# Kernel optimization log

Hardware: AMD Instinct MI355X
Metric: run time of the kernel (lower is better)

The kernel has to match this reference:

```python
import jax, jax.numpy as jnp
import numpy as np
import math

D_MODEL = 1024
NUM_HEADS = 16
BATCH = 2
SEQ = 2048

def setup_inputs() -> dict:
    key = jax.random.key(0)
    ks = jax.random.split(key, 9)
    s = 1.0 / math.sqrt(D_MODEL)
    inp = {
        "X": jax.random.normal(ks[0], (BATCH, SEQ, D_MODEL), dtype=jnp.float32),
        "Wq": jax.random.uniform(ks[1], (D_MODEL, D_MODEL), jnp.float32, -s, s),
        "bq": jax.random.uniform(ks[2], (D_MODEL,), jnp.float32, -s, s),
        "Wk": jax.random.uniform(ks[3], (D_MODEL, D_MODEL), jnp.float32, -s, s),
        "bk": jax.random.uniform(ks[4], (D_MODEL,), jnp.float32, -s, s),
        "Wv": jax.random.uniform(ks[5], (D_MODEL, D_MODEL), jnp.float32, -s, s),
        "bv": jax.random.uniform(ks[6], (D_MODEL,), jnp.float32, -s, s),
        "Wo": jax.random.uniform(ks[7], (D_MODEL, D_MODEL), jnp.float32, -s, s),
        "bo": jax.random.uniform(ks[8], (D_MODEL,), jnp.float32, -s, s),
    }
    return inp

def reference(X, Wq, bq, Wk, bk, Wv, bv, Wo, bo):
    B, S, D = X.shape
    H = NUM_HEADS
    dk = D // H
    # QKV projections (Linear: x @ W.T + b; here W stored as [in, out] so x @ W + b)
    q = X @ Wq + bq
    k = X @ Wk + bk
    v = X @ Wv + bv
    # split heads -> [B, H, S, dk]
    q = q.reshape(B, S, H, dk).transpose(0, 2, 1, 3)
    k = k.reshape(B, S, H, dk).transpose(0, 2, 1, 3)
    v = v.reshape(B, S, H, dk).transpose(0, 2, 1, 3)
    scores = jnp.einsum("bhqd,bhkd->bhqk", q, k) / math.sqrt(dk)
    weights = jax.nn.softmax(scores, axis=-1)
    attn = jnp.einsum("bhqk,bhkd->bhqd", weights, v)
    concat = attn.transpose(0, 2, 1, 3).reshape(B, S, D)
    return concat @ Wo + bo
```

## Files before the change

kernel.cpp:

```cpp
#include <hip/hip_runtime.h>
#include <stdint.h>

#define D_MODEL 1024
#define NH      16
#define DKH     64
#define BATCH   2
#define SEQ     2048
#define M_TOK   (BATCH*SEQ)

typedef __attribute__((ext_vector_type(8))) short bf16x8;
typedef __attribute__((ext_vector_type(4))) float f32x4;

__device__ __forceinline__ uint16_t f2b(float f) {
  uint32_t u = __builtin_bit_cast(uint32_t, f);
  return (uint16_t)((u + 0x7FFFu + ((u >> 16) & 1u)) >> 16);
}

__device__ __forceinline__ void gl2lds16(const uint16_t* g, uint16_t* l) {
  __builtin_amdgcn_global_load_lds(
      (const __attribute__((address_space(1))) void*)g,
      (__attribute__((address_space(3))) void*)l, 16, 0, 0);
}

__global__ void convx(const float* __restrict__ X, uint16_t* __restrict__ Xb) {
  int i = (blockIdx.x * 256 + threadIdx.x) * 8;
  float4 a = *(const float4*)(X + i);
  float4 b = *(const float4*)(X + i + 4);
  uint16_t tmp[8] = {f2b(a.x), f2b(a.y), f2b(a.z), f2b(a.w),
                     f2b(b.x), f2b(b.y), f2b(b.z), f2b(b.w)};
  *(uint4*)(Xb + i) = *(const uint4*)tmp;
}

__global__ void wtrans(const float* __restrict__ W0, const float* __restrict__ W1,
                       const float* __restrict__ W2, const float* __restrict__ W3,
                       uint16_t* __restrict__ T0, uint16_t* __restrict__ T1,
                       uint16_t* __restrict__ T2, uint16_t* __restrict__ T3) {
  __shared__ float tile[32][33];
  int z = blockIdx.z;
  const float* W = (z == 0) ? W0 : (z == 1) ? W1 : (z == 2) ? W2 : W3;
  uint16_t*    T = (z == 0) ? T0 : (z == 1) ? T1 : (z == 2) ? T2 : T3;
  int k0 = blockIdx.x * 32, n0 = blockIdx.y * 32;
  int tx = threadIdx.x, ty = threadIdx.y;
  tile[ty][tx] = W[(size_t)(k0 + ty) * D_MODEL + n0 + tx];
  __syncthreads();
  T[(size_t)(n0 + ty) * D_MODEL + k0 + tx] = f2b(tile[tx][ty]);
}

template <bool SWAP>
__device__ __forceinline__ void gemm_core(const uint16_t* __restrict__ A,
                                          const uint16_t* __restrict__ BT,
                                          uint16_t* As, uint16_t* Bs,
                                          int m0, int n0, int kBeg, int kEnd,
                                          f32x4 (&acc)[4][4]) {
  const int t    = threadIdx.x;
  const int lane = t & 63;
  const int qi   = lane & 15, g = lane >> 4;
  const int wm   = (t >> 7) & 1;
  const int wn   = (t >> 6) & 1;
  const int srow = t >> 2;
  const int sc   = (t & 3) ^ ((t >> 3) & 3);
  const int wbase = t & 192;
  const int rch  = (g ^ ((qi >> 1) & 3)) * 8;

  const uint16_t* Ag = A  + (size_t)(m0 + srow) * D_MODEL + sc * 8;
  const uint16_t* Bg = BT + (size_t)(n0 + srow) * D_MODEL + sc * 8;

#pragma unroll
  for (int j = 0; j < 2; j++) {
    gl2lds16(Ag + (size_t)j * 64 * D_MODEL + kBeg, As + (j * 256 + wbase) * 8);
    gl2lds16(Bg + (size_t)j * 64 * D_MODEL + kBeg, Bs + (j * 256 + wbase) * 8);
  }

  int cur = 0;
  for (int k0 = kBeg; k0 < kEnd; k0 += 32) {
    __syncthreads();
    int kn = k0 + 32;
    if (kn < kEnd) {
      int nb = (cur ^ 1) * 4096;
#pragma unroll
      for (int j = 0; j < 2; j++) {
        gl2lds16(Ag + (size_t)j * 64 * D_MODEL + kn, As + nb + (j * 256 + wbase) * 8);
        gl2lds16(Bg + (size_t)j * 64 * D_MODEL + kn, Bs + nb + (j * 256 + wbase) * 8);
      }
    }
    const uint16_t* Ab = As + cur * 4096;
    const uint16_t* Bb = Bs + cur * 4096;
    bf16x8 af[4], bf[4];
#pragma unroll
    for (int i = 0; i < 4; i++) {
      af[i] = *(const bf16x8*)(Ab + (wm * 64 + i * 16 + qi) * 32 + rch);
      bf[i] = *(const bf16x8*)(Bb + (wn * 64 + i * 16 + qi) * 32 + rch);
    }
#pragma unroll
    for (int i = 0; i < 4; i++)
#pragma unroll
      for (int j = 0; j < 4; j++)
        acc[i][j] = SWAP
          ? __builtin_amdgcn_mfma_f32_16x16x32_bf16(bf[j], af[i], acc[i][j], 0, 0, 0)
          : __builtin_amdgcn_mfma_f32_16x16x32_bf16(af[i], bf[j], acc[i][j], 0, 0, 0);
    cur ^= 1;
  }
}

__global__ __launch_bounds__(256) void qkv_gemm(
    const uint16_t* __restrict__ Xb,
    const uint16_t* __restrict__ WqT, const uint16_t* __restrict__ WkT,
    const uint16_t* __restrict__ WvT,
    const float* __restrict__ bq, const float* __restrict__ bk,
    const float* __restrict__ bv,
    uint16_t* __restrict__ Qo, uint16_t* __restrict__ Ko, uint16_t* __restrict__ Vt) {
  __shared__ __align__(16) uint16_t smem[17408];
  uint16_t* As = smem;
  uint16_t* Bs = smem + 8192;
  uint16_t* T  = smem;
  const int z = blockIdx.z;
  const uint16_t* BT  = (z == 0) ? WqT : (z == 1) ? WkT : WvT;
  const float*   bias = (z == 0) ? bq  : (z == 1) ? bk  : bv;
  const int m0 = blockIdx.y * 128, n0 = blockIdx.x * 128;
  const int lane = threadIdx.x & 63, qi = lane & 15, g = lane >> 4;
  const int wm = (threadIdx.x >> 7) & 1, wn = (threadIdx.x >> 6) & 1;
  const float l2e = 1.4426950408889634f * 0.125f;

  const f32x4 ZERO = {0.f, 0.f, 0.f, 0.f};
  f32x4 acc[4][4];
#pragma unroll
  for (int i = 0; i < 4; i++)
#pragma unroll
    for (int j = 0; j < 4; j++) acc[i][j] = ZERO;

  if (z == 2) {
    gemm_core<false>(Xb, BT, As, Bs, m0, n0, 0, D_MODEL, acc);
    __syncthreads();
#pragma unroll
    for (int i = 0; i < 4; i++) {
      int tok = wm * 64 + i * 16 + g * 4;
#pragma unroll
      for (int j = 0; j < 4; j++) {
        int ch = wn * 64 + j * 16 + qi;
        float bb = bias[n0 + ch];
        uint32_t lo = (uint32_t)f2b(acc[i][j][0] + bb) | ((uint32_t)f2b(acc[i][j][1] + bb) << 16);
        uint32_t hi = (uint32_t)f2b(acc[i][j][2] + bb) | ((uint32_t)f2b(acc[i][j][3] + bb) << 16);
        uint2 pk = {lo, hi};
        *(uint2*)(T + ch * 136 + tok) = pk;
      }
    }
    __syncthreads();
    {
      int ch = threadIdx.x >> 1, sh = threadIdx.x & 1;
      const uint16_t* src = T + ch * 136 + sh * 64;
      int bidx = m0 >> 11;
      uint16_t* dst = Vt + ((size_t)(bidx * D_MODEL + n0 + ch)) * SEQ + (m0 & 2047) + sh * 64;
#pragma unroll
      for (int u = 0; u < 8; u++)
        *(uint4*)(dst + u * 8) = *(const uint4*)(src + u * 8);
    }
  } else {
    gemm_core<true>(Xb, BT, As, Bs, m0, n0, 0, D_MODEL, acc);
    uint16_t* O = z ? Ko : Qo;
    const float osc = (z == 0) ? l2e : 1.0f;
#pragma unroll
    for (int i = 0; i < 4; i++) {
      size_t tok = m0 + wm * 64 + i * 16 + qi;
#pragma unroll
      for (int j = 0; j < 4; j++) {
        int ch = n0 + wn * 64 + j * 16 + g * 4;
        float4 bb = *(const float4*)(bias + ch);
        uint32_t lo = (uint32_t)f2b((acc[i][j][0] + bb.x) * osc) |
                      ((uint32_t)f2b((acc[i][j][1] + bb.y) * osc) << 16);
        uint32_t hi = (uint32_t)f2b((acc[i][j][2] + bb.z) * osc) |
                      ((uint32_t)f2b((acc[i][j][3] + bb.w) * osc) << 16);
        uint2 pk = {lo, hi};
        *(uint2*)(O + tok * D_MODEL + ch) = pk;
      }
    }
  }
}

__global__ __launch_bounds__(256) void oproj_gemm(
    const uint16_t* __restrict__ Ab, const uint16_t* __restrict__ WoT,
    const float* __restrict__ bo, float* __restrict__ out) {
  __shared__ __align__(16) uint16_t As[8192];
  __shared__ __align__(16) uint16_t Bs[4096];
  const int t = threadIdx.x;
  const int lane = t & 63, qi = lane & 15, g = lane >> 4;
  const int wm = (t >> 7) & 1;
  const int wn = (t >> 6) & 1;
  const int srow = t >> 2;
  const int sc = (t & 3) ^ ((t >> 3) & 3);
  const int wbase = t & 192;
  const int rch = (g ^ ((qi >> 1) & 3)) * 8;
  const int m0 = blockIdx.y * 128, n0 = blockIdx.x * 64;

  const uint16_t* Ag = Ab  + (size_t)(m0 + srow) * D_MODEL + sc * 8;
  const uint16_t* Bg = WoT + (size_t)(n0 + srow) * D_MODEL + sc * 8;

  const f32x4 ZERO = {0.f, 0.f, 0.f, 0.f};
  f32x4 acc[4][2];
#pragma unroll
  for (int i = 0; i < 4; i++)
#pragma unroll
    for (int j = 0; j < 2; j++) acc[i][j] = ZERO;

  gl2lds16(Ag, As + wbase * 8);
  gl2lds16(Ag + (size_t)64 * D_MODEL, As + (256 + wbase) * 8);
  gl2lds16(Bg, Bs + wbase * 8);

  int cur = 0;
  for (int k0 = 0; k0 < D_MODEL; k0 += 32) {
    __syncthreads();
    int kn = k0 + 32;
    if (kn < D_MODEL) {
      int nbA = (cur ^ 1) * 4096, nbB = (cur ^ 1) * 2048;
      gl2lds16(Ag + kn, As + nbA + wbase * 8);
      gl2lds16(Ag + (size_t)64 * D_MODEL + kn, As + nbA + (256 + wbase) * 8);
      gl2lds16(Bg + kn, Bs + nbB + wbase * 8);
    }
    const uint16_t* Abuf = As + cur * 4096;
    const uint16_t* Bbuf = Bs + cur * 2048;
    bf16x8 af[4], bf[2];
#pragma unroll
    for (int i = 0; i < 4; i++)
      af[i] = *(const bf16x8*)(Abuf + (wm * 64 + i * 16 + qi) * 32 + rch);
#pragma unroll
    for (int j = 0; j < 2; j++)
      bf[j] = *(const bf16x8*)(Bbuf + (wn * 32 + j * 16 + qi) * 32 + rch);
#pragma unroll
    for (int i = 0; i < 4; i++)
#pragma unroll
      for (int j = 0; j < 2; j++)
        acc[i][j] = __builtin_amdgcn_mfma_f32_16x16x32_bf16(bf[j], af[i], acc[i][j], 0, 0, 0);
    cur ^= 1;
  }

#pragma unroll
  for (int i = 0; i < 4; i++) {
    size_t tok = m0 + wm * 64 + i * 16 + qi;
#pragma unroll
    for (int j = 0; j < 2; j++) {
      int ch = n0 + wn * 32 + j * 16 + g * 4;
      float4 bb = *(const float4*)(bo + ch);
      float4 o = {acc[i][j][0] + bb.x, acc[i][j][1] + bb.y,
                  acc[i][j][2] + bb.z, acc[i][j][3] + bb.w};
      *(float4*)(out + tok * D_MODEL + ch) = o;
    }
  }
}

__global__ __launch_bounds__(512, 2) void attn_fwd(
    const uint16_t* __restrict__ Q, const uint16_t* __restrict__ K,
    const uint16_t* __restrict__ Vt, uint16_t* __restrict__ O) {
  __shared__ __align__(16) uint16_t sm[32768];
  uint16_t* Ps = sm + 16384;

  const int t = threadIdx.x, lane = t & 63, w = t >> 6;
  const int g = lane >> 4, qi = lane & 15;
  const int rch = (g ^ ((qi >> 1) & 3)) * 8;
  const int key = qi & 7;
  const int q0 = blockIdx.y * 256;
  const int bh = blockIdx.x, b = bh >> 4, h = bh & 15;
  const uint16_t* Qp = Q + (size_t)b * SEQ * D_MODEL + h * DKH;
  const uint16_t* Kp = K + (size_t)b * SEQ * D_MODEL + h * DKH;
  const uint16_t* Vp = Vt + (size_t)bh * DKH * SEQ;

  const int tt = t & 255, hs = t >> 8;
  const int srow = tt >> 2;
  const int sc = (tt & 3) ^ ((tt >> 3) & 3);
  const int wbase = tt & 192;

  bf16x8 qf[2][2];
#pragma unroll
  for (int i = 0; i < 2; i++) {
    const uint16_t* Qr = Qp + (size_t)(q0 + w * 32 + i * 16 + qi) * D_MODEL + g * 8;
    qf[0][i] = *(const bf16x8*)(Qr);
    qf[1][i] = *(const bf16x8*)(Qr + 32);
  }

  gl2lds16(Kp + (size_t)srow * D_MODEL + hs * 32 + sc * 8,
           sm + hs * 2048 + wbase * 8);
  gl2lds16(Vp + (size_t)srow * SEQ + hs * 32 + sc * 8,
           sm + 8192 + hs * 2048 + wbase * 8);
  __syncthreads();

  float lsum[2] = {0.f, 0.f};
  const f32x4 ZERO = {0.f, 0.f, 0.f, 0.f};
  f32x4 oaccT[4][2];
#pragma unroll
  for (int d = 0; d < 4; d++)
#pragma unroll
    for (int i = 0; i < 2; i++) oaccT[d][i] = ZERO;

  int cur = 0;
  for (int kt = 0; kt < SEQ / 64; kt++) {
    if (kt + 1 < SEQ / 64) {
      int nb = (cur ^ 1) * 4096;
      gl2lds16(Kp + (size_t)((kt + 1) * 64 + srow) * D_MODEL + hs * 32 + sc * 8,
               sm + nb + hs * 2048 + wbase * 8);
      gl2lds16(Vp + (size_t)srow * SEQ + (kt + 1) * 64 + hs * 32 + sc * 8,
               sm + 8192 + nb + hs * 2048 + wbase * 8);
    }
    const uint16_t* Kb = sm + cur * 4096;
    const uint16_t* Vb = sm + 8192 + cur * 4096;

    f32x4 sacc[4][2];
#pragma unroll
    for (int j = 0; j < 4; j++)
#pragma unroll
      for (int i = 0; i < 2; i++) sacc[j][i] = ZERO;
#pragma unroll
    for (int ks = 0; ks < 2; ks++) {
      const uint16_t* Ksb = Kb + ks * 2048;
      bf16x8 kf[4];
#pragma unroll
      for (int j = 0; j < 4; j++)
        kf[j] = *(const bf16x8*)(Ksb + (j * 16 + qi) * 32 + rch);
      __builtin_amdgcn_s_setprio(1);
#pragma unroll
      for (int j = 0; j < 4; j++)
#pragma unroll
        for (int i = 0; i < 2; i++)
          sacc[j][i] = __builtin_amdgcn_mfma_f32_16x16x32_bf16(kf[j], qf[ks][i], sacc[j][i], 0, 0, 0);
      __builtin_amdgcn_s_setprio(0);
    }

#pragma unroll
    for (int i = 0; i < 2; i++) {
      uint16_t* Pr = Ps + (w * 32 + i * 16 + qi) * 64;
#pragma unroll
      for (int j = 0; j < 4; j++) {
        float p0 = __builtin_amdgcn_exp2f(sacc[j][i][0]);
        float p1 = __builtin_amdgcn_exp2f(sacc[j][i][1]);
        float p2 = __builtin_amdgcn_exp2f(sacc[j][i][2]);
        float p3 = __builtin_amdgcn_exp2f(sacc[j][i][3]);
        lsum[i] += (p0 + p1) + (p2 + p3);
        uint2 pk = {__builtin_amdgcn_perm(__builtin_bit_cast(uint32_t, p1),
                                          __builtin_bit_cast(uint32_t, p0), 0x07060302u),
                    __builtin_amdgcn_perm(__builtin_bit_cast(uint32_t, p3),
                                          __builtin_bit_cast(uint32_t, p2), 0x07060302u)};
        *(uint2*)(Pr + (((j * 4 + g) ^ (2 * key)) << 2)) = pk;
      }
    }

#pragma unroll
    for (int ks = 0; ks < 2; ks++) {
      const uint16_t* Vsb = Vb + ks * 2048;
      bf16x8 vf[4], pf[2];
#pragma unroll
      for (int d = 0; d < 4; d++)
        vf[d] = *(const bf16x8*)(Vsb + (d * 16 + qi) * 32 + rch);
#pragma unroll
      for (int i = 0; i < 2; i++)
        pf[i] = *(const bf16x8*)(Ps + (w * 32 + i * 16 + qi) * 64 +
                                 (((ks * 4 + g) ^ key) << 3));
      __builtin_amdgcn_s_setprio(1);
#pragma unroll
      for (int d = 0; d < 4; d++)
#pragma unroll
        for (int i = 0; i < 2; i++)
          oaccT[d][i] = __builtin_amdgcn_mfma_f32_16x16x32_bf16(vf[d], pf[i], oaccT[d][i], 0, 0, 0);
      __builtin_amdgcn_s_setprio(0);
    }

    if (kt + 1 < SEQ / 64) __syncthreads();
    cur ^= 1;
  }

#pragma unroll
  for (int i = 0; i < 2; i++) {
    lsum[i] += __shfl_xor(lsum[i], 16, 64);
    lsum[i] += __shfl_xor(lsum[i], 32, 64);
  }
  float rl[2] = {1.f / lsum[0], 1.f / lsum[1]};

#pragma unroll
  for (int i = 0; i < 2; i++) {
    size_t row = (size_t)b * SEQ + q0 + w * 32 + i * 16 + qi;
#pragma unroll
    for (int d = 0; d < 4; d++) {
      uint32_t lo = (uint32_t)f2b(oaccT[d][i][0] * rl[i]) |
                    ((uint32_t)f2b(oaccT[d][i][1] * rl[i]) << 16);
      uint32_t hi = (uint32_t)f2b(oaccT[d][i][2] * rl[i]) |
                    ((uint32_t)f2b(oaccT[d][i][3] * rl[i]) << 16);
      uint2 pk = {lo, hi};
      *(uint2*)(O + row * D_MODEL + h * DKH + d * 16 + g * 4) = pk;
    }
  }
}

extern "C" void kernel_launch(void* const* d_in, const int* in_sizes, int n_in,
                              void* d_out, int out_size, void* d_ws, size_t ws_size,
                              hipStream_t stream) {
  (void)in_sizes; (void)n_in; (void)out_size; (void)ws_size;
  const float* X  = (const float*)d_in[0];
  const float* Wq = (const float*)d_in[1];
  const float* bq = (const float*)d_in[2];
  const float* Wk = (const float*)d_in[3];
  const float* bk = (const float*)d_in[4];
  const float* Wv = (const float*)d_in[5];
  const float* bv = (const float*)d_in[6];
  const float* Wo = (const float*)d_in[7];
  const float* bo = (const float*)d_in[8];
  float* out = (float*)d_out;

  char* p = (char*)d_ws;
  uint16_t* Xb  = (uint16_t*)p; p += (size_t)M_TOK * D_MODEL * 2;
  uint16_t* WqT = (uint16_t*)p; p += (size_t)D_MODEL * D_MODEL * 2;
  uint16_t* WkT = (uint16_t*)p; p += (size_t)D_MODEL * D_MODEL * 2;
  uint16_t* WvT = (uint16_t*)p; p += (size_t)D_MODEL * D_MODEL * 2;
  uint16_t* WoT = (uint16_t*)p; p += (size_t)D_MODEL * D_MODEL * 2;
  uint16_t* Qw  = (uint16_t*)p; p += (size_t)M_TOK * D_MODEL * 2;
  uint16_t* Kw  = (uint16_t*)p; p += (size_t)M_TOK * D_MODEL * 2;
  uint16_t* Vt  = (uint16_t*)p; p += (size_t)M_TOK * D_MODEL * 2;
  uint16_t* Ob  = (uint16_t*)p; p += (size_t)M_TOK * D_MODEL * 2;

  convx<<<(M_TOK * D_MODEL) / (256 * 8), 256, 0, stream>>>(X, Xb);
  wtrans<<<dim3(32, 32, 4), dim3(32, 32), 0, stream>>>(Wq, Wk, Wv, Wo, WqT, WkT, WvT, WoT);
  qkv_gemm<<<dim3(8, 32, 3), 256, 0, stream>>>(Xb, WqT, WkT, WvT, bq, bk, bv, Qw, Kw, Vt);
  attn_fwd<<<dim3(BATCH * NH, SEQ / 256), 512, 0, stream>>>(Qw, Kw, Vt, Ob);
  oproj_gemm<<<dim3(16, 32), 256, 0, stream>>>(Ob, WoT, bo, out);
}
```

Baseline: 192.1 us.

## Software-pipeline attention loop (PV of previous tile with QK of current) and fuse prep kernels

Restructures the attention main loop so each iteration runs the P·V MFMAs for the previous key tile before the QK^T and softmax for the current tile. V moves to a triple buffer so its tile stays live one extra iteration, which raises LDS use. The aim is to overlap the exp and P-store work with matrix-core work and cut pipeline bubbles. It also merges the X conversion and weight transpose kernels into a single launch, using float4 loads for the transpose.

```diff
diff --git a/kernel.cpp b/kernel.cpp
--- a/kernel.cpp
+++ b/kernel.cpp
@@ -22,28 +22,37 @@
       (__attribute__((address_space(3))) void*)l, 16, 0, 0);
 }
 
-__global__ void convx(const float* __restrict__ X, uint16_t* __restrict__ Xb) {
-  int i = (blockIdx.x * 256 + threadIdx.x) * 8;
-  float4 a = *(const float4*)(X + i);
-  float4 b = *(const float4*)(X + i + 4);
-  uint16_t tmp[8] = {f2b(a.x), f2b(a.y), f2b(a.z), f2b(a.w),
-                     f2b(b.x), f2b(b.y), f2b(b.z), f2b(b.w)};
-  *(uint4*)(Xb + i) = *(const uint4*)tmp;
-}
-
-__global__ void wtrans(const float* __restrict__ W0, const float* __restrict__ W1,
-                       const float* __restrict__ W2, const float* __restrict__ W3,
-                       uint16_t* __restrict__ T0, uint16_t* __restrict__ T1,
-                       uint16_t* __restrict__ T2, uint16_t* __restrict__ T3) {
-  __shared__ float tile[32][33];
-  int z = blockIdx.z;
-  const float* W = (z == 0) ? W0 : (z == 1) ? W1 : (z == 2) ? W2 : W3;
-  uint16_t*    T = (z == 0) ? T0 : (z == 1) ? T1 : (z == 2) ? T2 : T3;
-  int k0 = blockIdx.x * 32, n0 = blockIdx.y * 32;
-  int tx = threadIdx.x, ty = threadIdx.y;
-  tile[ty][tx] = W[(size_t)(k0 + ty) * D_MODEL + n0 + tx];
-  __syncthreads();
-  T[(size_t)(n0 + ty) * D_MODEL + k0 + tx] = f2b(tile[tx][ty]);
+__global__ __launch_bounds__(256) void prep(
+    const float* __restrict__ X, uint16_t* __restrict__ Xb,
+    const float* __restrict__ W0, const float* __restrict__ W1,
+    const float* __restrict__ W2, const float* __restrict__ W3,
+    uint16_t* __restrict__ T0, uint16_t* __restrict__ T1,
+    uint16_t* __restrict__ T2, uint16_t* __restrict__ T3) {
+  const int bid = blockIdx.x;
+  if (bid < 2048) {
+    int i = (bid * 256 + threadIdx.x) * 8;
+    float4 a = *(const float4*)(X + i);
+    float4 b = *(const float4*)(X + i + 4);
+    uint16_t tmp[8] = {f2b(a.x), f2b(a.y), f2b(a.z), f2b(a.w),
+                       f2b(b.x), f2b(b.y), f2b(b.z), f2b(b.w)};
+    *(uint4*)(Xb + i) = *(const uint4*)tmp;
+  } else {
+    __shared__ float tile[32][33];
+    int r = bid - 2048;
+    int z = r >> 10, tt = r & 1023;
+    const float* W = (z == 0) ? W0 : (z == 1) ? W1 : (z == 2) ? W2 : W3;
+    uint16_t*    T = (z == 0) ? T0 : (z == 1) ? T1 : (z == 2) ? T2 : T3;
+    int k0 = (tt & 31) * 32, n0 = (tt >> 5) * 32;
+    int t = threadIdx.x;
+    int rr = t >> 3, c4 = (t & 7) * 4;
+    float4 v = *(const float4*)(W + (size_t)(k0 + rr) * D_MODEL + n0 + c4);
+    tile[rr][c4] = v.x; tile[rr][c4 + 1] = v.y;
+    tile[rr][c4 + 2] = v.z; tile[rr][c4 + 3] = v.w;
+    __syncthreads();
+    uint16_t o[4] = {f2b(tile[c4][rr]), f2b(tile[c4 + 1][rr]),
+                     f2b(tile[c4 + 2][rr]), f2b(tile[c4 + 3][rr])};
+    *(uint2*)(T + (size_t)(n0 + rr) * D_MODEL + k0 + c4) = *(const uint2*)o;
+  }
 }
 
 template <bool SWAP>
@@ -249,8 +258,8 @@
 __global__ __launch_bounds__(512, 2) void attn_fwd(
     const uint16_t* __restrict__ Q, const uint16_t* __restrict__ K,
     const uint16_t* __restrict__ Vt, uint16_t* __restrict__ O) {
-  __shared__ __align__(16) uint16_t sm[32768];
-  uint16_t* Ps = sm + 16384;
+  __shared__ __align__(16) uint16_t sm[36864];
+  uint16_t* const Ps = sm + 20480;
 
   const int t = threadIdx.x, lane = t & 63, w = t >> 6;
   const int g = lane >> 4, qi = lane & 15;
@@ -275,11 +284,12 @@
     qf[1][i] = *(const bf16x8*)(Qr + 32);
   }
 
-  gl2lds16(Kp + (size_t)srow * D_MODEL + hs * 32 + sc * 8,
-           sm + hs * 2048 + wbase * 8);
-  gl2lds16(Vp + (size_t)srow * SEQ + hs * 32 + sc * 8,
-           sm + 8192 + hs * 2048 + wbase * 8);
-  __syncthreads();
+  auto STAGE = [&](int tile, uint16_t* kb, uint16_t* vb) {
+    gl2lds16(Kp + (size_t)(tile * 64 + srow) * D_MODEL + hs * 32 + sc * 8,
+             kb + hs * 2048 + wbase * 8);
+    gl2lds16(Vp + (size_t)srow * SEQ + tile * 64 + hs * 32 + sc * 8,
+             vb + hs * 2048 + wbase * 8);
+  };
 
   float lsum[2] = {0.f, 0.f};
   const f32x4 ZERO = {0.f, 0.f, 0.f, 0.f};
@@ -289,18 +299,7 @@
 #pragma unroll
     for (int i = 0; i < 2; i++) oaccT[d][i] = ZERO;
 
-  int cur = 0;
-  for (int kt = 0; kt < SEQ / 64; kt++) {
-    if (kt + 1 < SEQ / 64) {
-      int nb = (cur ^ 1) * 4096;
-      gl2lds16(Kp + (size_t)((kt + 1) * 64 + srow) * D_MODEL + hs * 32 + sc * 8,
-               sm + nb + hs * 2048 + wbase * 8);
-      gl2lds16(Vp + (size_t)srow * SEQ + (kt + 1) * 64 + hs * 32 + sc * 8,
-               sm + 8192 + nb + hs * 2048 + wbase * 8);
-    }
-    const uint16_t* Kb = sm + cur * 4096;
-    const uint16_t* Vb = sm + 8192 + cur * 4096;
-
+  auto QK_SM = [&](const uint16_t* Kb) {
     f32x4 sacc[4][2];
 #pragma unroll
     for (int j = 0; j < 4; j++)
@@ -321,7 +320,6 @@
           sacc[j][i] = __builtin_amdgcn_mfma_f32_16x16x32_bf16(kf[j], qf[ks][i], sacc[j][i], 0, 0, 0);
       __builtin_amdgcn_s_setprio(0);
     }
-
 #pragma unroll
     for (int i = 0; i < 2; i++) {
       uint16_t* Pr = Ps + (w * 32 + i * 16 + qi) * 64;
@@ -339,7 +337,9 @@
         *(uint2*)(Pr + (((j * 4 + g) ^ (2 * key)) << 2)) = pk;
       }
     }
-
+  };
+
+  auto PV = [&](const uint16_t* Vb) {
 #pragma unroll
     for (int ks = 0; ks < 2; ks++) {
       const uint16_t* Vsb = Vb + ks * 2048;
@@ -359,10 +359,25 @@
           oaccT[d][i] = __builtin_amdgcn_mfma_f32_16x16x32_bf16(vf[d], pf[i], oaccT[d][i], 0, 0, 0);
       __builtin_amdgcn_s_setprio(0);
     }
-
+  };
+
+  STAGE(0, sm, sm + 8192);
+  STAGE(1, sm + 4096, sm + 8192 + 4096);
+  __syncthreads();
+  QK_SM(sm);
+  __syncthreads();
+
+  for (int kt = 1; kt < SEQ / 64; kt++) {
+    if (kt + 1 < SEQ / 64)
+      STAGE(kt + 1, sm + ((kt + 1) & 1) * 4096,
+            sm + 8192 + ((kt + 1) % 3) * 4096);
+    const uint16_t* Kb = sm + (kt & 1) * 4096;
+    const uint16_t* Vb = sm + 8192 + ((kt - 1) % 3) * 4096;
+    PV(Vb);
+    QK_SM(Kb);
     if (kt + 1 < SEQ / 64) __syncthreads();
-    cur ^= 1;
-  }
+  }
+  PV(sm + 8192 + ((SEQ / 64 - 1) % 3) * 4096);
 
 #pragma unroll
   for (int i = 0; i < 2; i++) {
@@ -412,8 +427,7 @@
   uint16_t* Vt  = (uint16_t*)p; p += (size_t)M_TOK * D_MODEL * 2;
   uint16_t* Ob  = (uint16_t*)p; p += (size_t)M_TOK * D_MODEL * 2;
 
-  convx<<<(M_TOK * D_MODEL) / (256 * 8), 256, 0, stream>>>(X, Xb);
-  wtrans<<<dim3(32, 32, 4), dim3(32, 32), 0, stream>>>(Wq, Wk, Wv, Wo, WqT, WkT, WvT, WoT);
+  prep<<<6144, 256, 0, stream>>>(X, Xb, Wq, Wk, Wv, Wo, WqT, WkT, WvT, WoT);
   qkv_gemm<<<dim3(8, 32, 3), 256, 0, stream>>>(Xb, WqT, WkT, WvT, bq, bk, bv, Qw, Kw, Vt);
   attn_fwd<<<dim3(BATCH * NH, SEQ / 256), 512, 0, stream>>>(Qw, Kw, Vt, Ob);
   oproj_gemm<<<dim3(16, 32), 256, 0, stream>>>(Ob, WoT, bo, out);
```

After: 191.3 us. Within noise of the previous version (-0.4%).
